# Optimization experiments

Hardware: AMD Instinct MI355X
Metric: run time of the kernel (lower is better)

Reference implementation:

```python
import jax, jax.numpy as jnp
import numpy as np

QMAX = 127.0   # 8-bit symmetric quantization
BN_EPS = 1e-5
MID = 576      # in_channels * 6 expansion


def act_fake_quant(x):
    """Per-tensor symmetric 8-bit fake-quant of activations (HAWQ QuantAct).
    Returns dequantized value and the scaling factor. STE for gradients."""
    s = jax.lax.stop_gradient(jnp.max(jnp.abs(x)) / QMAX + 1e-8)
    q = jnp.clip(jnp.round(x / s), -QMAX, QMAX) * s
    return x + jax.lax.stop_gradient(q - x), s


def fold_bn(w, gamma, beta, mean, var):
    """Fold BN into conv weights/bias (QuantBnConv2d.set_param math)."""
    f = gamma / jnp.sqrt(var + BN_EPS)
    return w * f[:, None, None, None], beta - mean * f


def weight_fake_quant(w):
    """Per-output-channel symmetric 8-bit fake-quant of folded weights."""
    s = jax.lax.stop_gradient(jnp.max(jnp.abs(w), axis=(1, 2, 3)) / QMAX + 1e-8)
    sb = s[:, None, None, None]
    q = jnp.clip(jnp.round(w / sb), -QMAX, QMAX) * sb
    return w + jax.lax.stop_gradient(q - w), s


def qbn_conv(x, w, gamma, beta, mean, var, stride, groups, pad):
    """BN-folded, weight-quantized conv (QuantBnConv2d forward)."""
    wf, bf = fold_bn(w, gamma, beta, mean, var)
    wq, ws = weight_fake_quant(wf)
    y = jax.lax.conv_general_dilated(
        x, wq, window_strides=(stride, stride), padding=pad,
        dimension_numbers=('NCHW', 'OIHW', 'NCHW'), feature_group_count=groups)
    return y + bf[None, :, None, None], ws


def setup_inputs() -> dict:
    key = jax.random.key(0)
    ks = jax.random.split(key, 16)
    C_in, C_out = 96, 96
    d = {'x': jax.random.normal(ks[0], (64, C_in, 28, 28), jnp.float32)}
    def bn(k, c):
        k1, k2, k3, k4 = jax.random.split(k, 4)
        return (1.0 + 0.1 * jax.random.normal(k1, (c,), jnp.float32),   # gamma
                0.1 * jax.random.normal(k2, (c,), jnp.float32),          # beta
                0.1 * jax.random.normal(k3, (c,), jnp.float32),          # running mean
                0.5 + jax.random.uniform(k4, (c,), jnp.float32))         # running var
    # conv1: 1x1 expansion 96 -> 576
    d['w1'] = 0.1 * jax.random.normal(ks[1], (MID, C_in, 1, 1), jnp.float32)
    d['g1'], d['b1'], d['m1'], d['v1'] = bn(ks[2], MID)
    # conv2: 3x3 depthwise, groups=576
    d['w2'] = 0.1 * jax.random.normal(ks[3], (MID, 1, 3, 3), jnp.float32)
    d['g2'], d['b2'], d['m2'], d['v2'] = bn(ks[4], MID)
    # conv3: 1x1 projection 576 -> 96
    d['w3'] = 0.1 * jax.random.normal(ks[5], (C_out, MID, 1, 1), jnp.float32)
    d['g3'], d['b3'], d['m3'], d['v3'] = bn(ks[6], C_out)
    return d


def reference(x, w1, g1, b1, m1, v1, w2, g2, b2, m2, v2, w3, g3, b3, m3, v3):
    identity = x
    # quant_act on input
    y, act_sf = act_fake_quant(x)
    # conv1 (1x1 expansion) + ReLU6 + quant_act1
    y, _ = qbn_conv(y, w1, g1, b1, m1, v1, stride=1, groups=1, pad='VALID')
    y = jnp.clip(y, 0.0, 6.0)
    y, _ = act_fake_quant(y)
    # conv2 (3x3 depthwise) + ReLU6 + quant_act2
    y, _ = qbn_conv(y, w2, g2, b2, m2, v2, stride=1, groups=MID,
                    pad=((1, 1), (1, 1)))
    y = jnp.clip(y, 0.0, 6.0)
    y, _ = act_fake_quant(y)
    # conv3 (1x1 projection, linear)
    y, _ = qbn_conv(y, w3, g3, b3, m3, v3, stride=1, groups=1, pad='VALID')
    # residual add + quant_act_int32 requantization
    y = y + identity
    y, out_sf = act_fake_quant(y)
    return y, out_sf
```

## Files before the change

kernel.cpp:

```cpp
#include <hip/hip_runtime.h>
#include <hip/hip_fp16.h>

#define CIN   96
#define MIDC  576
#define COUT  96
#define HW    784
#define W28   28
#define NX    4816896

typedef __attribute__((ext_vector_type(8))) short short8;
typedef __attribute__((ext_vector_type(4))) float floatx4;


__device__ __forceinline__ float wave_max64(float v){
  #pragma unroll
  for(int i=32;i>=1;i>>=1) v = fmaxf(v, __shfl_xor(v, i, 64));
  return v;
}

__device__ __forceinline__ void block_max_atomic(float v, unsigned* dst){
  v = wave_max64(v);
  __shared__ float sm[8];
  int lane = threadIdx.x & 63, w = threadIdx.x >> 6;
  if(lane==0) sm[w] = v;
  __syncthreads();
  if(threadIdx.x==0){
    int nw = (blockDim.x + 63) >> 6;
    float m = sm[0];
    for(int i=1;i<nw;i++) m = fmaxf(m, sm[i]);
    atomicMax(dst, __float_as_uint(m));
  }
}

__device__ __forceinline__ float fq(float x, float s){
  float q = rintf(x / s);
  q = fminf(fmaxf(q, -127.f), 127.f);
  return q * s;
}

__device__ __forceinline__ float qint(float x, float s){
  return fminf(fmaxf(rintf(x / s), -127.f), 127.f);
}

__device__ __forceinline__ ushort f2bf(float f){
  return (ushort)(__float_as_uint(f) >> 16);
}


__global__ __launch_bounds__(256) void k_prep(
    const float* __restrict__ w1,const float* __restrict__ g1,const float* __restrict__ b1,const float* __restrict__ m1,const float* __restrict__ v1,
    const float* __restrict__ w2,const float* __restrict__ g2,const float* __restrict__ b2,const float* __restrict__ m2,const float* __restrict__ v2,
    const float* __restrict__ w3,const float* __restrict__ g3,const float* __restrict__ b3,const float* __restrict__ m3,const float* __restrict__ v3,
    ushort* __restrict__ qw1, float* __restrict__ sc1, float* __restrict__ bq1,
    float*  __restrict__ wq2, float* __restrict__ bq2,
    ushort* __restrict__ qw3, float* __restrict__ sc3, float* __restrict__ bq3,
    const float4* __restrict__ xv, unsigned* umax)
{
  int b = blockIdx.x, tid = threadIdx.x;
  if(b >= 1248){
    float m = 0.f;
    for(int i = (b-1248)*256 + tid; i < NX/4; i += 512*256){
      float4 v = xv[i];
      m = fmaxf(m, fmaxf(fmaxf(fabsf(v.x), fabsf(v.y)), fmaxf(fabsf(v.z), fabsf(v.w))));
    }
    block_max_atomic(m, umax);
    return;
  }
  if(tid >= 64) return;
  int lane = tid;
  if(b < MIDC){
    int o = b;
    float f = g1[o] / sqrtf(v1[o] + 1e-5f);
    float x0 = w1[o*CIN + lane] * f;
    float x1 = (lane < 32) ? w1[o*CIN + 64 + lane] * f : 0.f;
    float m = wave_max64(fmaxf(fabsf(x0), fabsf(x1)));
    float s = m / 127.f + 1e-8f;
    qw1[o*CIN + lane] = f2bf(qint(x0, s));
    if(lane < 32) qw1[o*CIN + 64 + lane] = f2bf(qint(x1, s));
    if(lane==0){ sc1[o] = s; bq1[o] = b1[o] - m1[o]*f; }
  } else if(b < 2*MIDC){
    int c = b - MIDC;
    float f = g2[c] / sqrtf(v2[c] + 1e-5f);
    float x0 = (lane < 9) ? w2[c*9 + lane] * f : 0.f;
    float m = wave_max64(fabsf(x0));
    float s = m / 127.f + 1e-8f;
    if(lane < 9) wq2[c*9 + lane] = fq(x0, s);
    if(lane==0) bq2[c] = b2[c] - m2[c]*f;
  } else {
    int o = b - 2*MIDC;
    float f = g3[o] / sqrtf(v3[o] + 1e-5f);
    float xs[9]; float m = 0.f;
    #pragma unroll
    for(int k=0;k<9;k++){ int c = lane + 64*k; xs[k] = w3[o*MIDC + c] * f; m = fmaxf(m, fabsf(xs[k])); }
    m = wave_max64(m);
    float s = m / 127.f + 1e-8f;
    #pragma unroll
    for(int k=0;k<9;k++){ int c = lane + 64*k; qw3[o*MIDC + c] = f2bf(qint(xs[k], s)); }
    if(lane==0){ sc3[o] = s; bq3[o] = b3[o] - m3[o]*f; }
  }
}

__global__ __launch_bounds__(256) void k_quantxT(const float* __restrict__ x,
    const unsigned* __restrict__ umax, ushort* __restrict__ qxT)
{
  __shared__ ushort lds[56*100];
  int n = blockIdx.x, pc = blockIdx.y, tid = threadIdx.x;
  float s0 = __uint_as_float(umax[0])/127.f + 1e-8f;
  for(int i = tid; i < 96*56; i += 256){
    int c = i/56, p = i - c*56;
    float v = x[(size_t)(n*CIN + c)*HW + pc*56 + p];
    lds[p*100 + c] = f2bf(qint(v, s0));
  }
  __syncthreads();
  const uint* lu = (const uint*)lds;
  for(int i = tid; i < 56*12; i += 256){
    int r = i/12, cb = i - r*12;
    const uint* lr = lu + r*50 + cb*4;
    uint4 v; v.x = lr[0]; v.y = lr[1]; v.z = lr[2]; v.w = lr[3];
    *(uint4*)(qxT + ((size_t)(n*12 + cb)*HW + pc*56 + r)*8) = v;
  }
}

__global__ __launch_bounds__(256) void k_conv1(const ushort* __restrict__ qxT,
    const ushort* __restrict__ qw1, const float* __restrict__ sc1, const float* __restrict__ bq1,
    unsigned* umax, __half* __restrict__ y1T)
{
  int n = blockIdx.x, mt = blockIdx.y;
  int w = threadIdx.x >> 6, l = threadIdx.x & 63;
  int lhi = l >> 4, llo = l & 15;
  int m0 = mt*64 + w*16;
  float s0 = __uint_as_float(umax[0])/127.f + 1e-8f;
  short8 a[3];
  #pragma unroll
  for(int ks=0; ks<3; ks++)
    a[ks] = *(const short8*)(qw1 + (m0 + llo)*CIN + ks*32 + lhi*8);
  float scf[4], bf[4];
  #pragma unroll
  for(int r=0;r<4;r++){ int o = m0 + lhi*4 + r; scf[r] = s0*sc1[o]; bf[r] = bq1[o]; }
  int cgbase = (m0 >> 3) + (lhi >> 1);
  int c8base = (lhi & 1) * 4;
  float tmax = 0.f;
  for(int ch=0; ch<7; ch++){
    int p0 = ch*112;
    floatx4 acc[7];
    #pragma unroll
    for(int f=0;f<7;f++) acc[f] = (floatx4){0.f,0.f,0.f,0.f};
    #pragma unroll
    for(int ks=0; ks<3; ks++){
      #pragma unroll
      for(int f=0; f<7; f++){
        const short8 b = *(const short8*)(qxT + ((size_t)(n*12 + ks*4 + lhi)*HW + p0 + f*16 + llo)*8);
        acc[f] = __builtin_amdgcn_mfma_f32_16x16x32_bf16(a[ks], b, acc[f], 0, 0, 0);
      }
    }
    #pragma unroll
    for(int f=0; f<7; f++){
      uint pk0 = 0, pk1 = 0;
      #pragma unroll
      for(int r=0;r<4;r++){
        float v = fmaf(acc[f][r], scf[r], bf[r]);
        v = fminf(fmaxf(v, 0.f), 6.f);
        tmax = fmaxf(tmax, v);
        uint hb = (uint)__half_as_ushort(__float2half(v));
        if(r==0) pk0 = hb;        else if(r==1) pk0 |= hb<<16;
        else if(r==2) pk1 = hb;   else pk1 |= hb<<16;
      }
      uint2 pk; pk.x = pk0; pk.y = pk1;
      *(uint2*)((ushort*)y1T + ((size_t)(n*72 + cgbase)*HW + p0 + f*16 + llo)*8 + c8base) = pk;
    }
  }
  block_max_atomic(tmax, umax + 1);
}

__global__ __launch_bounds__(256) void k_conv2(const __half* __restrict__ y1T,
    const float* __restrict__ wq2, const float* __restrict__ bq2,
    unsigned* umax, __half* __restrict__ y2T)
{
  __shared__ ushort tile[2][30*30*8];
  int cg = blockIdx.x >> 4, nb = (blockIdx.x & 15) << 2;
  int tid = threadIdx.x;
  float s1 = __uint_as_float(umax[1])/127.f + 1e-8f;
  float r1 = 1.f/s1;
  const float* wc = wq2 + cg*72;
  const float* bc = bq2 + cg*8;
  float tmax = 0.f;

  #pragma unroll
  for(int bfi=0; bfi<2; bfi++){
    uint4* t4z = (uint4*)tile[bfi];
    if(tid < 116){
      int h, w;
      if(tid < 30){ h = 0; w = tid; }
      else if(tid < 60){ h = 29; w = tid - 30; }
      else if(tid < 88){ h = tid - 59; w = 0; }
      else { h = tid - 87; w = 29; }
      t4z[h*30 + w] = (uint4){0u,0u,0u,0u};
    }
  }

  uint4 ld[4];
  {
    const uint4* g4 = (const uint4*)(y1T + (size_t)(nb*72 + cg)*HW*8);
    #pragma unroll
    for(int i=0;i<4;i++){ int p = tid + i*256; if(p < HW) ld[i] = g4[p]; }
    uint4* t4 = (uint4*)tile[0];
    #pragma unroll
    for(int i=0;i<4;i++){
      int p = tid + i*256;
      if(p < HW){
        int h = p/W28, w = p - h*W28;
        uint rw[4] = {ld[i].x, ld[i].y, ld[i].z, ld[i].w};
        uint pk[4];
        #pragma unroll
        for(int j=0;j<4;j++){
          float lo = __half2float(__ushort_as_half((ushort)(rw[j] & 0xffffu)));
          float hi = __half2float(__ushort_as_half((ushort)(rw[j] >> 16)));
          uint qlo = (uint)__half_as_ushort(__float2half(rintf(lo * r1)));
          uint qhi = (uint)__half_as_ushort(__float2half(rintf(hi * r1)));
          pk[j] = (qhi << 16) | qlo;
        }
        t4[(h+1)*30 + (w+1)] = (uint4){pk[0], pk[1], pk[2], pk[3]};
      }
    }
  }

  int cur = 0;
  for(int it=0; it<4; it++){
    int n = nb + it;
    if(it < 3){
      const uint4* g4 = (const uint4*)(y1T + (size_t)((n+1)*72 + cg)*HW*8);
      #pragma unroll
      for(int i=0;i<4;i++){ int p = tid + i*256; if(p < HW) ld[i] = g4[p]; }
    }
    __syncthreads();
    const uint4* t4 = (const uint4*)tile[cur];
    uint4* o4 = (uint4*)(y2T + (size_t)(n*72 + cg)*HW*8);
    #pragma unroll
    for(int i=0;i<4;i++){
      int p = tid + i*256;
      if(p < HW){
        int h = p/W28, w = p - h*W28;
        float acc[8];
        #pragma unroll
        for(int c=0;c<8;c++) acc[c] = 0.f;
        #pragma unroll
        for(int dy=0; dy<3; dy++){
          #pragma unroll
          for(int dx=0; dx<3; dx++){
            uint4 v = t4[(h+dy)*30 + (w+dx)];
            uint rw[4] = {v.x, v.y, v.z, v.w};
            #pragma unroll
            for(int j=0;j<4;j++){
              float lo = __half2float(__ushort_as_half((ushort)(rw[j] & 0xffffu)));
              float hi = __half2float(__ushort_as_half((ushort)(rw[j] >> 16)));
              acc[2*j]   = fmaf(lo, wc[(2*j)*9   + dy*3 + dx], acc[2*j]);
              acc[2*j+1] = fmaf(hi, wc[(2*j+1)*9 + dy*3 + dx], acc[2*j+1]);
            }
          }
        }
        uint pk[4];
        #pragma unroll
        for(int j=0;j<4;j++){
          float o0 = fmaf(acc[2*j],   s1, bc[2*j]);
          float o1 = fmaf(acc[2*j+1], s1, bc[2*j+1]);
          o0 = fminf(fmaxf(o0, 0.f), 6.f);
          o1 = fminf(fmaxf(o1, 0.f), 6.f);
          tmax = fmaxf(tmax, fmaxf(o0, o1));
          uint lo = (uint)__half_as_ushort(__float2half(o0));
          uint hi = (uint)__half_as_ushort(__float2half(o1));
          pk[j] = (hi << 16) | lo;
        }
        o4[p] = (uint4){pk[0], pk[1], pk[2], pk[3]};
      }
    }
    if(it < 3){
      uint4* t4n = (uint4*)tile[cur ^ 1];
      #pragma unroll
      for(int i=0;i<4;i++){
        int p = tid + i*256;
        if(p < HW){
          int h = p/W28, w = p - h*W28;
          uint rw[4] = {ld[i].x, ld[i].y, ld[i].z, ld[i].w};
          uint pk[4];
          #pragma unroll
          for(int j=0;j<4;j++){
            float lo = __half2float(__ushort_as_half((ushort)(rw[j] & 0xffffu)));
            float hi = __half2float(__ushort_as_half((ushort)(rw[j] >> 16)));
            uint qlo = (uint)__half_as_ushort(__float2half(rintf(lo * r1)));
            uint qhi = (uint)__half_as_ushort(__float2half(rintf(hi * r1)));
            pk[j] = (qhi << 16) | qlo;
          }
          t4n[(h+1)*30 + (w+1)] = (uint4){pk[0], pk[1], pk[2], pk[3]};
        }
      }
    }
    cur ^= 1;
  }
  block_max_atomic(tmax, umax + 2);
}

__global__ __launch_bounds__(384) void k_conv3(const __half* __restrict__ y2T,
    const ushort* __restrict__ qw3, const float* __restrict__ sc3, const float* __restrict__ bq3,
    const float* __restrict__ x, unsigned* umax, float* __restrict__ out)
{
  __shared__ ushort lds[24*64*8];
  int n = blockIdx.x, pc = blockIdx.y, tid = threadIdx.x;
  int w = tid >> 6, l = tid & 63;
  int lhi = l >> 4, llo = l & 15;
  int m0 = w*16;
  int p0 = pc*56;
  float s2 = __uint_as_float(umax[2])/127.f + 1e-8f;
  uint4* l4 = (uint4*)lds;
  if(tid < 192){
    int cl = tid >> 3, px = 56 + (tid & 7);
    l4[cl*64 + px] = (uint4){0u,0u,0u,0u};
  }
  float scf[4], bf[4];
  #pragma unroll
  for(int r=0;r<4;r++){ int o = m0 + lhi*4 + r; scf[r] = s2*sc3[o]; bf[r] = bq3[o]; }
  floatx4 acc[4];
  #pragma unroll
  for(int f=0;f<4;f++) acc[f] = (floatx4){0.f,0.f,0.f,0.f};
  for(int ck=0; ck<3; ck++){
    __syncthreads();
    for(int i = tid; i < 24*56; i += 384){
      int cl = i/56, r = i - cl*56;
      uint4 v = *(const uint4*)((const ushort*)y2T + ((size_t)(n*72 + ck*24 + cl)*HW + p0 + r)*8);
      uint rw[4] = {v.x, v.y, v.z, v.w};
      uint pk[4];
      #pragma unroll
      for(int j=0;j<4;j++){
        float lo = __half2float(__ushort_as_half((ushort)(rw[j] & 0xffffu)));
        float hi = __half2float(__ushort_as_half((ushort)(rw[j] >> 16)));
        uint qlo = (uint)f2bf(rintf(lo / s2));
        uint qhi = (uint)f2bf(rintf(hi / s2));
        pk[j] = (qhi << 16) | qlo;
      }
      uint4 sv; sv.x = pk[0]; sv.y = pk[1]; sv.z = pk[2]; sv.w = pk[3];
      l4[cl*64 + r] = sv;
    }
    __syncthreads();
    #pragma unroll
    for(int ks=0; ks<6; ks++){
      const short8 a = *(const short8*)(qw3 + (m0 + llo)*MIDC + ck*192 + ks*32 + lhi*8);
      #pragma unroll
      for(int f=0; f<4; f++){
        const short8 b = *(const short8*)(lds + ((ks*4 + lhi)*64 + f*16 + llo)*8);
        acc[f] = __builtin_amdgcn_mfma_f32_16x16x32_bf16(a, b, acc[f], 0, 0, 0);
      }
    }
  }
  float tmax = 0.f;
  #pragma unroll
  for(int f=0; f<4; f++){
    if(f*16 + llo < 56){
      #pragma unroll
      for(int r=0;r<4;r++){
        size_t idx = (size_t)(n*COUT + m0 + lhi*4 + r)*HW + p0 + f*16 + llo;
        float v = fmaf(acc[f][r], scf[r], bf[r]) + x[idx];
        tmax = fmaxf(tmax, fabsf(v));
        out[idx] = v;
      }
    }
  }
  block_max_atomic(tmax, umax + 3);
}

__global__ void k_finalq(float* __restrict__ out, const unsigned* __restrict__ umax, float* __restrict__ sf){
  int i = blockIdx.x*256 + threadIdx.x;
  float s3 = __uint_as_float(umax[3]) / 127.f + 1e-8f;
  float4* o4 = (float4*)out;
  float4 v = o4[i];
  v.x = fq(v.x, s3); v.y = fq(v.y, s3); v.z = fq(v.z, s3); v.w = fq(v.w, s3);
  o4[i] = v;
  if(i == 0) *sf = s3;
}


extern "C" void kernel_launch(void* const* d_in, const int* in_sizes, int n_in,
                              void* d_out, int out_size, void* d_ws, size_t ws_size,
                              hipStream_t stream)
{
  const float* x  = (const float*)d_in[0];
  const float* w1 = (const float*)d_in[1];
  const float* g1 = (const float*)d_in[2];
  const float* b1 = (const float*)d_in[3];
  const float* m1 = (const float*)d_in[4];
  const float* v1 = (const float*)d_in[5];
  const float* w2 = (const float*)d_in[6];
  const float* g2 = (const float*)d_in[7];
  const float* b2 = (const float*)d_in[8];
  const float* m2 = (const float*)d_in[9];
  const float* v2 = (const float*)d_in[10];
  const float* w3 = (const float*)d_in[11];
  const float* g3 = (const float*)d_in[12];
  const float* b3 = (const float*)d_in[13];
  const float* m3 = (const float*)d_in[14];
  const float* v3 = (const float*)d_in[15];

  char* ws = (char*)d_ws;
  unsigned* umax = (unsigned*)(ws + 0);
  float* sc1  = (float*)(ws + 256);
  float* bq1  = (float*)(ws + 2560);
  float* bq2  = (float*)(ws + 4864);
  float* wq2  = (float*)(ws + 7168);
  float* sc3  = (float*)(ws + 27904);
  float* bq3  = (float*)(ws + 28288);
  ushort* qw1 = (ushort*)(ws + 28672);
  ushort* qw3 = (ushort*)(ws + 139264);
  ushort* qxT = (ushort*)(ws + 249856);
  __half* y1T  = (__half*)(ws + 9883648);
  __half* y2T  = (__half*)(ws + 67686400);

  float* outp = (float*)d_out;

  hipMemsetAsync(umax, 0, 16, stream);
  k_prep<<<1760, 256, 0, stream>>>(w1,g1,b1,m1,v1, w2,g2,b2,m2,v2, w3,g3,b3,m3,v3,
                                   qw1,sc1,bq1, wq2,bq2, qw3,sc3,bq3,
                                   (const float4*)x, umax);
  k_quantxT<<<dim3(64,14), 256, 0, stream>>>(x, umax, qxT);
  k_conv1<<<dim3(64,9), 256, 0, stream>>>(qxT, qw1, sc1, bq1, umax, y1T);
  k_conv2<<<1152, 256, 0, stream>>>(y1T, wq2, bq2, umax, y2T);
  k_conv3<<<dim3(64,14), 384, 0, stream>>>(y2T, qw3, sc3, bq3, x, umax, outp);
  k_finalq<<<NX/4/256, 256, 0, stream>>>(outp, umax, outp + NX);
}
```

Before: 136.4 us.

## Fuse depthwise conv into projection GEMM with max-only conv2 pass

Stops writing the depthwise output y2T to global memory. A lightweight k_conv2m pass now computes the depthwise conv only to find the activation max. k_conv3f then recomputes the depthwise conv per tile straight into LDS, quantizes it, and feeds the MFMA projection. This trades about 58 MB of y2 write and read traffic for running the depthwise arithmetic twice. It also splits conv1 across a z-dimension of 2 for more blocks, and replaces divides with reciprocal multiplies in quantization, which can change rounding slightly.

```diff
diff --git a/kernel.cpp b/kernel.cpp
--- a/kernel.cpp
+++ b/kernel.cpp
@@ -42,8 +42,53 @@
   return fminf(fmaxf(rintf(x / s), -127.f), 127.f);
 }
 
+__device__ __forceinline__ float qintr(float x, float r){
+  return fminf(fmaxf(rintf(x * r), -127.f), 127.f);
+}
+
 __device__ __forceinline__ ushort f2bf(float f){
   return (ushort)(__float_as_uint(f) >> 16);
+}
+
+__device__ __forceinline__ void dw_quad(const ushort* __restrict__ base, int h, int k,
+    float r1, const float* wf, float acc[4][8])
+{
+  #pragma unroll
+  for(int p=0;p<4;p++)
+    #pragma unroll
+    for(int c=0;c<8;c++) acc[p][c] = 0.f;
+  #pragma unroll
+  for(int dy=0; dy<3; dy++){
+    int hh = h + dy - 1;
+    bool rok = (hh >= 0) && (hh < 28);
+    int hc = rok ? hh : 0;
+    uint4 row[6];
+    #pragma unroll
+    for(int dc=0; dc<6; dc++){
+      int ww = 4*k + dc - 1;
+      bool cok = (ww >= 0) && (ww < 28);
+      int wc2 = cok ? ww : 0;
+      uint4 v = *(const uint4*)(base + (hc*W28 + wc2)*8);
+      if(!(rok && cok)){ v.x = 0u; v.y = 0u; v.z = 0u; v.w = 0u; }
+      row[dc] = v;
+    }
+    #pragma unroll
+    for(int c=0; c<8; c++){
+      float q[6];
+      #pragma unroll
+      for(int dc=0; dc<6; dc++){
+        uint u = ((const uint*)&row[dc])[c>>1];
+        ushort hb = (c&1) ? (ushort)(u >> 16) : (ushort)(u & 0xffffu);
+        q[dc] = rintf(__half2float(__ushort_as_half(hb)) * r1);
+      }
+      float w0 = wf[c*9 + dy*3 + 0];
+      float w1 = wf[c*9 + dy*3 + 1];
+      float w2 = wf[c*9 + dy*3 + 2];
+      #pragma unroll
+      for(int p=0;p<4;p++)
+        acc[p][c] = fmaf(q[p], w0, fmaf(q[p+1], w1, fmaf(q[p+2], w2, acc[p][c])));
+    }
+  }
 }
 
 
@@ -106,10 +151,11 @@
   __shared__ ushort lds[56*100];
   int n = blockIdx.x, pc = blockIdx.y, tid = threadIdx.x;
   float s0 = __uint_as_float(umax[0])/127.f + 1e-8f;
+  float r0 = 1.f/s0;
   for(int i = tid; i < 96*56; i += 256){
     int c = i/56, p = i - c*56;
     float v = x[(size_t)(n*CIN + c)*HW + pc*56 + p];
-    lds[p*100 + c] = f2bf(qint(v, s0));
+    lds[p*100 + c] = f2bf(qintr(v, r0));
   }
   __syncthreads();
   const uint* lu = (const uint*)lds;
@@ -126,6 +172,7 @@
     unsigned* umax, __half* __restrict__ y1T)
 {
   int n = blockIdx.x, mt = blockIdx.y;
+  int ch0 = blockIdx.z * 4, ch1 = blockIdx.z ? 7 : 4;
   int w = threadIdx.x >> 6, l = threadIdx.x & 63;
   int lhi = l >> 4, llo = l & 15;
   int m0 = mt*64 + w*16;
@@ -140,7 +187,7 @@
   int cgbase = (m0 >> 3) + (lhi >> 1);
   int c8base = (lhi & 1) * 4;
   float tmax = 0.f;
-  for(int ch=0; ch<7; ch++){
+  for(int ch=ch0; ch<ch1; ch++){
     int p0 = ch*112;
     floatx4 acc[7];
     #pragma unroll
@@ -172,181 +219,107 @@
   block_max_atomic(tmax, umax + 1);
 }
 
-__global__ __launch_bounds__(256) void k_conv2(const __half* __restrict__ y1T,
-    const float* __restrict__ wq2, const float* __restrict__ bq2,
-    unsigned* umax, __half* __restrict__ y2T)
-{
-  __shared__ ushort tile[2][30*30*8];
-  int cg = blockIdx.x >> 4, nb = (blockIdx.x & 15) << 2;
+__global__ __launch_bounds__(256) void k_conv2m(const __half* __restrict__ y1T,
+    const float* __restrict__ wq2, const float* __restrict__ bq2, unsigned* umax)
+{
+  __shared__ float wls[72];
+  __shared__ float bls[8];
+  int cg = blockIdx.x % 72, nb = (blockIdx.x / 72) * 4;
   int tid = threadIdx.x;
   float s1 = __uint_as_float(umax[1])/127.f + 1e-8f;
   float r1 = 1.f/s1;
-  const float* wc = wq2 + cg*72;
-  const float* bc = bq2 + cg*8;
+  if(tid < 72) wls[tid] = wq2[cg*72 + tid] * s1;
+  if(tid >= 72 && tid < 80) bls[tid-72] = bq2[cg*8 + tid - 72];
+  __syncthreads();
   float tmax = 0.f;
-
-  #pragma unroll
-  for(int bfi=0; bfi<2; bfi++){
-    uint4* t4z = (uint4*)tile[bfi];
-    if(tid < 116){
-      int h, w;
-      if(tid < 30){ h = 0; w = tid; }
-      else if(tid < 60){ h = 29; w = tid - 30; }
-      else if(tid < 88){ h = tid - 59; w = 0; }
-      else { h = tid - 87; w = 29; }
-      t4z[h*30 + w] = (uint4){0u,0u,0u,0u};
-    }
-  }
-
-  uint4 ld[4];
-  {
-    const uint4* g4 = (const uint4*)(y1T + (size_t)(nb*72 + cg)*HW*8);
-    #pragma unroll
-    for(int i=0;i<4;i++){ int p = tid + i*256; if(p < HW) ld[i] = g4[p]; }
-    uint4* t4 = (uint4*)tile[0];
-    #pragma unroll
-    for(int i=0;i<4;i++){
-      int p = tid + i*256;
-      if(p < HW){
-        int h = p/W28, w = p - h*W28;
-        uint rw[4] = {ld[i].x, ld[i].y, ld[i].z, ld[i].w};
+  #pragma unroll
+  for(int it=0; it<4; it++){
+    int q = tid + it*256;
+    if(q < 784){
+      int kk = q % 7; int rest = q / 7;
+      int h = rest % 28; int n = nb + rest / 28;
+      const ushort* base = (const ushort*)y1T + (size_t)(n*72 + cg)*HW*8;
+      float a[4][8];
+      dw_quad(base, h, kk, r1, wls, a);
+      #pragma unroll
+      for(int p=0;p<4;p++)
+        #pragma unroll
+        for(int c=0;c<8;c++){
+          float v = fminf(fmaxf(a[p][c] + bls[c], 0.f), 6.f);
+          tmax = fmaxf(tmax, v);
+        }
+    }
+  }
+  block_max_atomic(tmax, umax + 2);
+}
+
+__global__ __launch_bounds__(384) void k_conv3f(const __half* __restrict__ y1T,
+    const float* __restrict__ wq2, const float* __restrict__ bq2,
+    const ushort* __restrict__ qw3, const float* __restrict__ sc3, const float* __restrict__ bq3,
+    const float* __restrict__ x, unsigned* umax, float* __restrict__ out)
+{
+  __shared__ ushort btile[24*64*8];
+  __shared__ float wls[MIDC*9];
+  __shared__ float bls[MIDC];
+  int n = blockIdx.x, pc = blockIdx.y, tid = threadIdx.x;
+  int w = tid >> 6, l = tid & 63;
+  int lhi = l >> 4, llo = l & 15;
+  int m0 = w*16, p0 = pc*56;
+  float s1 = __uint_as_float(umax[1])/127.f + 1e-8f;
+  float r1 = 1.f/s1;
+  float s2 = __uint_as_float(umax[2])/127.f + 1e-8f;
+  float r2 = 1.f/s2;
+  for(int i = tid; i < MIDC*9; i += 384) wls[i] = wq2[i] * s1;
+  for(int i = tid; i < MIDC; i += 384) bls[i] = bq2[i];
+  if(tid < 192){
+    int cl = tid >> 3, px = 56 + (tid & 7);
+    uint4 z; z.x=0u; z.y=0u; z.z=0u; z.w=0u;
+    *(uint4*)(btile + (cl*64 + px)*8) = z;
+  }
+  float scf[4], bfv[4];
+  #pragma unroll
+  for(int r=0;r<4;r++){ int o = m0 + lhi*4 + r; scf[r] = s2*sc3[o]; bfv[r] = bq3[o]; }
+  floatx4 acc[4];
+  #pragma unroll
+  for(int f=0;f<4;f++) acc[f] = (floatx4){0.f,0.f,0.f,0.f};
+
+  int cg_l = tid / 14, q14 = tid % 14;
+  int rr = q14 / 7, kk = q14 % 7;
+  bool active = tid < 336;
+  int h = 2*pc + rr;
+  int sp = rr*28 + kk*4;
+
+  for(int ck=0; ck<3; ck++){
+    __syncthreads();
+    if(active){
+      int cg = ck*24 + cg_l;
+      const ushort* base = (const ushort*)y1T + (size_t)(n*72 + cg)*HW*8;
+      float a[4][8];
+      dw_quad(base, h, kk, r1, wls + cg*72, a);
+      const float* bp = bls + cg*8;
+      #pragma unroll
+      for(int p=0;p<4;p++){
         uint pk[4];
         #pragma unroll
         for(int j=0;j<4;j++){
-          float lo = __half2float(__ushort_as_half((ushort)(rw[j] & 0xffffu)));
-          float hi = __half2float(__ushort_as_half((ushort)(rw[j] >> 16)));
-          uint qlo = (uint)__half_as_ushort(__float2half(rintf(lo * r1)));
-          uint qhi = (uint)__half_as_ushort(__float2half(rintf(hi * r1)));
-          pk[j] = (qhi << 16) | qlo;
+          float v0 = fminf(fmaxf(a[p][2*j]   + bp[2*j],   0.f), 6.f);
+          float v1 = fminf(fmaxf(a[p][2*j+1] + bp[2*j+1], 0.f), 6.f);
+          uint q0 = (uint)f2bf(rintf(v0 * r2));
+          uint q1 = (uint)f2bf(rintf(v1 * r2));
+          pk[j] = (q1 << 16) | q0;
         }
-        t4[(h+1)*30 + (w+1)] = (uint4){pk[0], pk[1], pk[2], pk[3]};
-      }
-    }
-  }
-
-  int cur = 0;
-  for(int it=0; it<4; it++){
-    int n = nb + it;
-    if(it < 3){
-      const uint4* g4 = (const uint4*)(y1T + (size_t)((n+1)*72 + cg)*HW*8);
-      #pragma unroll
-      for(int i=0;i<4;i++){ int p = tid + i*256; if(p < HW) ld[i] = g4[p]; }
+        uint4 sv; sv.x = pk[0]; sv.y = pk[1]; sv.z = pk[2]; sv.w = pk[3];
+        *(uint4*)(btile + ((cg_l*64) + sp + p)*8) = sv;
+      }
     }
     __syncthreads();
-    const uint4* t4 = (const uint4*)tile[cur];
-    uint4* o4 = (uint4*)(y2T + (size_t)(n*72 + cg)*HW*8);
-    #pragma unroll
-    for(int i=0;i<4;i++){
-      int p = tid + i*256;
-      if(p < HW){
-        int h = p/W28, w = p - h*W28;
-        float acc[8];
-        #pragma unroll
-        for(int c=0;c<8;c++) acc[c] = 0.f;
-        #pragma unroll
-        for(int dy=0; dy<3; dy++){
-          #pragma unroll
-          for(int dx=0; dx<3; dx++){
-            uint4 v = t4[(h+dy)*30 + (w+dx)];
-            uint rw[4] = {v.x, v.y, v.z, v.w};
-            #pragma unroll
-            for(int j=0;j<4;j++){
-              float lo = __half2float(__ushort_as_half((ushort)(rw[j] & 0xffffu)));
-              float hi = __half2float(__ushort_as_half((ushort)(rw[j] >> 16)));
-              acc[2*j]   = fmaf(lo, wc[(2*j)*9   + dy*3 + dx], acc[2*j]);
-              acc[2*j+1] = fmaf(hi, wc[(2*j+1)*9 + dy*3 + dx], acc[2*j+1]);
-            }
-          }
-        }
-        uint pk[4];
-        #pragma unroll
-        for(int j=0;j<4;j++){
-          float o0 = fmaf(acc[2*j],   s1, bc[2*j]);
-          float o1 = fmaf(acc[2*j+1], s1, bc[2*j+1]);
-          o0 = fminf(fmaxf(o0, 0.f), 6.f);
-          o1 = fminf(fmaxf(o1, 0.f), 6.f);
-          tmax = fmaxf(tmax, fmaxf(o0, o1));
-          uint lo = (uint)__half_as_ushort(__float2half(o0));
-          uint hi = (uint)__half_as_ushort(__float2half(o1));
-          pk[j] = (hi << 16) | lo;
-        }
-        o4[p] = (uint4){pk[0], pk[1], pk[2], pk[3]};
-      }
-    }
-    if(it < 3){
-      uint4* t4n = (uint4*)tile[cur ^ 1];
-      #pragma unroll
-      for(int i=0;i<4;i++){
-        int p = tid + i*256;
-        if(p < HW){
-          int h = p/W28, w = p - h*W28;
-          uint rw[4] = {ld[i].x, ld[i].y, ld[i].z, ld[i].w};
-          uint pk[4];
-          #pragma unroll
-          for(int j=0;j<4;j++){
-            float lo = __half2float(__ushort_as_half((ushort)(rw[j] & 0xffffu)));
-            float hi = __half2float(__ushort_as_half((ushort)(rw[j] >> 16)));
-            uint qlo = (uint)__half_as_ushort(__float2half(rintf(lo * r1)));
-            uint qhi = (uint)__half_as_ushort(__float2half(rintf(hi * r1)));
-            pk[j] = (qhi << 16) | qlo;
-          }
-          t4n[(h+1)*30 + (w+1)] = (uint4){pk[0], pk[1], pk[2], pk[3]};
-        }
-      }
-    }
-    cur ^= 1;
-  }
-  block_max_atomic(tmax, umax + 2);
-}
-
-__global__ __launch_bounds__(384) void k_conv3(const __half* __restrict__ y2T,
-    const ushort* __restrict__ qw3, const float* __restrict__ sc3, const float* __restrict__ bq3,
-    const float* __restrict__ x, unsigned* umax, float* __restrict__ out)
-{
-  __shared__ ushort lds[24*64*8];
-  int n = blockIdx.x, pc = blockIdx.y, tid = threadIdx.x;
-  int w = tid >> 6, l = tid & 63;
-  int lhi = l >> 4, llo = l & 15;
-  int m0 = w*16;
-  int p0 = pc*56;
-  float s2 = __uint_as_float(umax[2])/127.f + 1e-8f;
-  uint4* l4 = (uint4*)lds;
-  if(tid < 192){
-    int cl = tid >> 3, px = 56 + (tid & 7);
-    l4[cl*64 + px] = (uint4){0u,0u,0u,0u};
-  }
-  float scf[4], bf[4];
-  #pragma unroll
-  for(int r=0;r<4;r++){ int o = m0 + lhi*4 + r; scf[r] = s2*sc3[o]; bf[r] = bq3[o]; }
-  floatx4 acc[4];
-  #pragma unroll
-  for(int f=0;f<4;f++) acc[f] = (floatx4){0.f,0.f,0.f,0.f};
-  for(int ck=0; ck<3; ck++){
-    __syncthreads();
-    for(int i = tid; i < 24*56; i += 384){
-      int cl = i/56, r = i - cl*56;
-      uint4 v = *(const uint4*)((const ushort*)y2T + ((size_t)(n*72 + ck*24 + cl)*HW + p0 + r)*8);
-      uint rw[4] = {v.x, v.y, v.z, v.w};
-      uint pk[4];
-      #pragma unroll
-      for(int j=0;j<4;j++){
-        float lo = __half2float(__ushort_as_half((ushort)(rw[j] & 0xffffu)));
-        float hi = __half2float(__ushort_as_half((ushort)(rw[j] >> 16)));
-        uint qlo = (uint)f2bf(rintf(lo / s2));
-        uint qhi = (uint)f2bf(rintf(hi / s2));
-        pk[j] = (qhi << 16) | qlo;
-      }
-      uint4 sv; sv.x = pk[0]; sv.y = pk[1]; sv.z = pk[2]; sv.w = pk[3];
-      l4[cl*64 + r] = sv;
-    }
-    __syncthreads();
     #pragma unroll
     for(int ks=0; ks<6; ks++){
-      const short8 a = *(const short8*)(qw3 + (m0 + llo)*MIDC + ck*192 + ks*32 + lhi*8);
+      const short8 a8 = *(const short8*)(qw3 + (m0 + llo)*MIDC + ck*192 + ks*32 + lhi*8);
       #pragma unroll
       for(int f=0; f<4; f++){
-        const short8 b = *(const short8*)(lds + ((ks*4 + lhi)*64 + f*16 + llo)*8);
-        acc[f] = __builtin_amdgcn_mfma_f32_16x16x32_bf16(a, b, acc[f], 0, 0, 0);
+        const short8 b8 = *(const short8*)(btile + ((ks*4 + lhi)*64 + f*16 + llo)*8);
+        acc[f] = __builtin_amdgcn_mfma_f32_16x16x32_bf16(a8, b8, acc[f], 0, 0, 0);
       }
     }
   }
@@ -357,7 +330,7 @@
       #pragma unroll
       for(int r=0;r<4;r++){
         size_t idx = (size_t)(n*COUT + m0 + lhi*4 + r)*HW + p0 + f*16 + llo;
-        float v = fmaf(acc[f][r], scf[r], bf[r]) + x[idx];
+        float v = fmaf(acc[f][r], scf[r], bfv[r]) + x[idx];
         tmax = fmaxf(tmax, fabsf(v));
         out[idx] = v;
       }
@@ -409,8 +382,7 @@
   ushort* qw1 = (ushort*)(ws + 28672);
   ushort* qw3 = (ushort*)(ws + 139264);
   ushort* qxT = (ushort*)(ws + 249856);
-  __half* y1T  = (__half*)(ws + 9883648);
-  __half* y2T  = (__half*)(ws + 67686400);
+  __half* y1T = (__half*)(ws + 9883648);
 
   float* outp = (float*)d_out;
 
@@ -419,8 +391,8 @@
                                    qw1,sc1,bq1, wq2,bq2, qw3,sc3,bq3,
                                    (const float4*)x, umax);
   k_quantxT<<<dim3(64,14), 256, 0, stream>>>(x, umax, qxT);
-  k_conv1<<<dim3(64,9), 256, 0, stream>>>(qxT, qw1, sc1, bq1, umax, y1T);
-  k_conv2<<<1152, 256, 0, stream>>>(y1T, wq2, bq2, umax, y2T);
-  k_conv3<<<dim3(64,14), 384, 0, stream>>>(y2T, qw3, sc3, bq3, x, umax, outp);
+  k_conv1<<<dim3(64,9,2), 256, 0, stream>>>(qxT, qw1, sc1, bq1, umax, y1T);
+  k_conv2m<<<1152, 256, 0, stream>>>(y1T, wq2, bq2, umax);
+  k_conv3f<<<dim3(64,14), 384, 0, stream>>>(y1T, wq2, bq2, qw3, sc3, bq3, x, umax, outp);
   k_finalq<<<NX/4/256, 256, 0, stream>>>(outp, umax, outp + NX);
 }
```

After: 196.3 us. 43.9% more time.
